# Performance work log

Measured on AMD Instinct MI355X. Metric: run time of the kernel, lower is better.

The kernel has to match this reference:

```python
import jax, jax.numpy as jnp
import numpy as np

H = 2048
S = 8192

def setup_inputs() -> dict:
    key = jax.random.key(0)
    k1, k2, k3 = jax.random.split(key, 3)
    hidden = jax.random.normal(k1, (1, 1, H), dtype=jnp.float32)
    encoder_outputs = jax.random.normal(k2, (S, 1, H), dtype=jnp.float32)
    # nn.Linear(H, H): weight [H, H], bias [H]; Kaiming-uniform-ish scale
    bound = 1.0 / np.sqrt(H)
    W = jax.random.uniform(k3, (H, H), dtype=jnp.float32, minval=-bound, maxval=bound)
    b = jnp.zeros((H,), dtype=jnp.float32)
    return {"hidden": hidden, "encoder_outputs": encoder_outputs, "W": W, "b": b}

def reference(hidden, encoder_outputs, W, b):
    # hidden: [1,1,H] -> [H]; encoder_outputs: [S,1,H] -> [S,H]
    h = hidden[0, 0]
    enc = encoder_outputs[:, 0, :]
    # per-step: energy_i = W @ enc_i + b; score_i = h . energy_i  (vectorized)
    energies = jnp.einsum('sh,h->s', enc @ W.T + b, h)  # [S]
    attn = jax.nn.softmax(energies)  # softmax over seq dim (dim 0 of 1-D tensor)
    return attn[None, None, :]  # [1,1,S]
```

## Files before the change

### kernel.cpp

```cpp
#include <hip/hip_runtime.h>
#include <math.h>

#define H 2048
#define S 8192
#define JCHUNK 64

__global__ void wt_h_kernel(const float* __restrict__ W, const float* __restrict__ h,
                            float* __restrict__ u) {
    int k = blockIdx.x * blockDim.x + threadIdx.x;
    int j0 = blockIdx.y * JCHUNK;
    float acc = 0.f;
#pragma unroll 8
    for (int j = j0; j < j0 + JCHUNK; ++j) {
        acc += h[j] * W[(size_t)j * H + k];
    }
    atomicAdd(&u[k], acc);
}

__global__ void enc_dot_kernel(const float* __restrict__ enc, const float* __restrict__ u,
                               float* __restrict__ e) {
    int wave = threadIdx.x >> 6;
    int lane = threadIdx.x & 63;
    int s = blockIdx.x * 4 + wave;
    const float4* row = (const float4*)(enc + (size_t)s * H);
    const float4* u4  = (const float4*)u;
    float acc = 0.f;
#pragma unroll
    for (int i = lane; i < H / 4; i += 64) {
        float4 a = row[i];
        float4 b = u4[i];
        acc += a.x * b.x + a.y * b.y + a.z * b.z + a.w * b.w;
    }
#pragma unroll
    for (int off = 32; off > 0; off >>= 1) acc += __shfl_down(acc, off);
    if (lane == 0) e[s] = acc;
}

__global__ void softmax_kernel(const float* __restrict__ e, float* __restrict__ out) {
    __shared__ float red[16];
    __shared__ float bcast;
    int tid = threadIdx.x;
    int lane = tid & 63;
    int wv = tid >> 6;

    float vals[8];
    float m = -INFINITY;
#pragma unroll
    for (int i = 0; i < 8; ++i) {
        vals[i] = e[tid + i * 1024];
        m = fmaxf(m, vals[i]);
    }
#pragma unroll
    for (int off = 32; off > 0; off >>= 1) m = fmaxf(m, __shfl_down(m, off));
    if (lane == 0) red[wv] = m;
    __syncthreads();
    if (tid == 0) {
        float mm = red[0];
#pragma unroll
        for (int i = 1; i < 16; ++i) mm = fmaxf(mm, red[i]);
        bcast = mm;
    }
    __syncthreads();
    float M = bcast;

    float ssum = 0.f;
#pragma unroll
    for (int i = 0; i < 8; ++i) {
        vals[i] = __expf(vals[i] - M);
        ssum += vals[i];
    }
#pragma unroll
    for (int off = 32; off > 0; off >>= 1) ssum += __shfl_down(ssum, off);
    if (lane == 0) red[wv] = ssum;
    __syncthreads();
    if (tid == 0) {
        float t = 0.f;
#pragma unroll
        for (int i = 0; i < 16; ++i) t += red[i];
        bcast = t;
    }
    __syncthreads();
    float inv = 1.f / bcast;
#pragma unroll
    for (int i = 0; i < 8; ++i) out[tid + i * 1024] = vals[i] * inv;
}

extern "C" void kernel_launch(void* const* d_in, const int* in_sizes, int n_in,
                              void* d_out, int out_size, void* d_ws, size_t ws_size,
                              hipStream_t stream) {
    const float* hidden = (const float*)d_in[0];
    const float* enc    = (const float*)d_in[1];
    const float* W      = (const float*)d_in[2];
    float* out = (float*)d_out;

    float* u = (float*)d_ws;
    float* e = (float*)((char*)d_ws + H * sizeof(float));

    hipMemsetAsync(u, 0, H * sizeof(float), stream);

    dim3 g1(H / 256, H / JCHUNK);
    wt_h_kernel<<<g1, 256, 0, stream>>>(W, hidden, u);

    enc_dot_kernel<<<S / 4, 256, 0, stream>>>(enc, u, e);

    softmax_kernel<<<1, 1024, 0, stream>>>(e, out);
}
```

Measured before the change: 114.1 us.

## Fuse W^T h, encoder dot and softmax into one cooperative kernel

Replaces the three-kernel pipeline with a single cooperative kernel of 256 blocks that uses grid.sync between phases: computing W^T h with atomics, per-row dot products over the encoder outputs, and a two-pass softmax using per-block max and sum partials. Scores stay in registers, so there is no intermediate score buffer and two kernel launches go away. The single-block softmax becomes a distributed reduction. In exchange it adds three grid-wide barriers and runs only 256 blocks, which may limit the memory parallelism available for streaming the 64 MB encoder tensor.

```diff
diff --git a/kernel.cpp b/kernel.cpp
--- a/kernel.cpp
+++ b/kernel.cpp
@@ -1,88 +1,114 @@
 #include <hip/hip_runtime.h>
+#include <hip/hip_cooperative_groups.h>
 #include <math.h>
+
+namespace cg = cooperative_groups;
 
 #define H 2048
 #define S 8192
-#define JCHUNK 64
+#define NBLK 256
+#define NTHR 256
 
-__global__ void wt_h_kernel(const float* __restrict__ W, const float* __restrict__ h,
-                            float* __restrict__ u) {
-    int k = blockIdx.x * blockDim.x + threadIdx.x;
-    int j0 = blockIdx.y * JCHUNK;
-    float acc = 0.f;
-#pragma unroll 8
-    for (int j = j0; j < j0 + JCHUNK; ++j) {
-        acc += h[j] * W[(size_t)j * H + k];
+__global__ void __launch_bounds__(NTHR, 1) attn_fused(
+    const float* __restrict__ W, const float* __restrict__ h,
+    const float* __restrict__ enc, float* __restrict__ u,
+    float* __restrict__ blockred, float* __restrict__ out)
+{
+    cg::grid_group grid = cg::this_grid();
+    const int b = blockIdx.x, tid = threadIdx.x;
+    const int lane = tid & 63, wv = tid >> 6;
+
+    {
+        const int kt = b >> 7;
+        const int jc = b & 127;
+        const int j0 = jc * 16;
+        const int c4 = kt * 256 + tid;
+        const float4* W4 = (const float4*)W;
+        float4 acc = make_float4(0.f, 0.f, 0.f, 0.f);
+#pragma unroll
+        for (int jj = 0; jj < 16; ++jj) {
+            const int j = j0 + jj;
+            const float hj = h[j];
+            float4 w = W4[(size_t)j * 512 + c4];
+            acc.x += hj * w.x; acc.y += hj * w.y;
+            acc.z += hj * w.z; acc.w += hj * w.w;
+        }
+        atomicAdd(&u[c4 * 4 + 0], acc.x);
+        atomicAdd(&u[c4 * 4 + 1], acc.y);
+        atomicAdd(&u[c4 * 4 + 2], acc.z);
+        atomicAdd(&u[c4 * 4 + 3], acc.w);
     }
-    atomicAdd(&u[k], acc);
-}
+    grid.sync();
 
-__global__ void enc_dot_kernel(const float* __restrict__ enc, const float* __restrict__ u,
-                               float* __restrict__ e) {
-    int wave = threadIdx.x >> 6;
-    int lane = threadIdx.x & 63;
-    int s = blockIdx.x * 4 + wave;
-    const float4* row = (const float4*)(enc + (size_t)s * H);
-    const float4* u4  = (const float4*)u;
-    float acc = 0.f;
+    const int gw = b * 4 + wv;
+    const float4* enc4 = (const float4*)enc;
+    const float4* u4   = (const float4*)u;
+    float4 ur[8];
 #pragma unroll
-    for (int i = lane; i < H / 4; i += 64) {
-        float4 a = row[i];
-        float4 b = u4[i];
-        acc += a.x * b.x + a.y * b.y + a.z * b.z + a.w * b.w;
-    }
-#pragma unroll
-    for (int off = 32; off > 0; off >>= 1) acc += __shfl_down(acc, off);
-    if (lane == 0) e[s] = acc;
-}
+    for (int it = 0; it < 8; ++it) ur[it] = u4[lane + 64 * it];
 
-__global__ void softmax_kernel(const float* __restrict__ e, float* __restrict__ out) {
-    __shared__ float red[16];
-    __shared__ float bcast;
-    int tid = threadIdx.x;
-    int lane = tid & 63;
-    int wv = tid >> 6;
-
-    float vals[8];
+    float e[8];
     float m = -INFINITY;
 #pragma unroll
-    for (int i = 0; i < 8; ++i) {
-        vals[i] = e[tid + i * 1024];
-        m = fmaxf(m, vals[i]);
+    for (int r = 0; r < 8; ++r) {
+        const size_t s = (size_t)gw * 8 + r;
+        const float4* row = enc4 + s * 512;
+        float acc = 0.f;
+#pragma unroll
+        for (int it = 0; it < 8; ++it) {
+            float4 a = row[lane + 64 * it];
+            acc += a.x * ur[it].x + a.y * ur[it].y
+                 + a.z * ur[it].z + a.w * ur[it].w;
+        }
+#pragma unroll
+        for (int off = 32; off > 0; off >>= 1) acc += __shfl_xor(acc, off);
+        e[r] = acc;
+        m = fmaxf(m, acc);
     }
+    __shared__ float sred[4];
+    __shared__ float sbc;
+    if (lane == 0) sred[wv] = m;
+    __syncthreads();
+    if (tid == 0)
+        blockred[b] = fmaxf(fmaxf(sred[0], sred[1]), fmaxf(sred[2], sred[3]));
+    grid.sync();
+
+    {
+        float v = (tid < NBLK) ? blockred[tid] : -INFINITY;
 #pragma unroll
-    for (int off = 32; off > 0; off >>= 1) m = fmaxf(m, __shfl_down(m, off));
-    if (lane == 0) red[wv] = m;
+        for (int off = 32; off > 0; off >>= 1) v = fmaxf(v, __shfl_xor(v, off));
+        if (lane == 0) sred[wv] = v;
+        __syncthreads();
+        if (tid == 0)
+            sbc = fmaxf(fmaxf(sred[0], sred[1]), fmaxf(sred[2], sred[3]));
+        __syncthreads();
+    }
+    const float M = sbc;
+    float p[8];
+    float ls = 0.f;
+#pragma unroll
+    for (int r = 0; r < 8; ++r) { p[r] = __expf(e[r] - M); ls += p[r]; }
     __syncthreads();
-    if (tid == 0) {
-        float mm = red[0];
+    if (lane == 0) sred[wv] = ls;
+    __syncthreads();
+    if (tid == 0)
+        blockred[NBLK + b] = sred[0] + sred[1] + sred[2] + sred[3];
+    grid.sync();
+
+    {
+        float v = (tid < NBLK) ? blockred[NBLK + tid] : 0.f;
 #pragma unroll
-        for (int i = 1; i < 16; ++i) mm = fmaxf(mm, red[i]);
-        bcast = mm;
+        for (int off = 32; off > 0; off >>= 1) v += __shfl_xor(v, off);
+        if (lane == 0) sred[wv] = v;
+        __syncthreads();
+        if (tid == 0) sbc = sred[0] + sred[1] + sred[2] + sred[3];
+        __syncthreads();
     }
-    __syncthreads();
-    float M = bcast;
-
-    float ssum = 0.f;
+    const float inv = 1.f / sbc;
+    float tmp = 0.f;
 #pragma unroll
-    for (int i = 0; i < 8; ++i) {
-        vals[i] = __expf(vals[i] - M);
-        ssum += vals[i];
-    }
-#pragma unroll
-    for (int off = 32; off > 0; off >>= 1) ssum += __shfl_down(ssum, off);
-    if (lane == 0) red[wv] = ssum;
-    __syncthreads();
-    if (tid == 0) {
-        float t = 0.f;
-#pragma unroll
-        for (int i = 0; i < 16; ++i) t += red[i];
-        bcast = t;
-    }
-    __syncthreads();
-    float inv = 1.f / bcast;
-#pragma unroll
-    for (int i = 0; i < 8; ++i) out[tid + i * 1024] = vals[i] * inv;
+    for (int r = 0; r < 8; ++r) if (lane == r) tmp = p[r] * inv;
+    if (lane < 8) out[(size_t)gw * 8 + lane] = tmp;
 }
 
 extern "C" void kernel_launch(void* const* d_in, const int* in_sizes, int n_in,
@@ -93,15 +119,13 @@
     const float* W      = (const float*)d_in[2];
     float* out = (float*)d_out;
 
-    float* u = (float*)d_ws;
-    float* e = (float*)((char*)d_ws + H * sizeof(float));
+    float* u        = (float*)d_ws;
+    float* blockred = (float*)((char*)d_ws + H * sizeof(float));
 
     hipMemsetAsync(u, 0, H * sizeof(float), stream);
 
-    dim3 g1(H / 256, H / JCHUNK);
-    wt_h_kernel<<<g1, 256, 0, stream>>>(W, hidden, u);
-
-    enc_dot_kernel<<<S / 4, 256, 0, stream>>>(enc, u, e);
-
-    softmax_kernel<<<1, 1024, 0, stream>>>(e, out);
+    void* args[] = {(void*)&W, (void*)&hidden, (void*)&enc,
+                    (void*)&u, (void*)&blockred, (void*)&out};
+    hipLaunchCooperativeKernel((void*)attn_fused, dim3(NBLK), dim3(NTHR),
+                               args, 0, stream);
 }
```

Result: slower. 224.2 us (+96.5%).
